# Kernel tuning notes

Hardware: AMD Instinct MI355X
Metric: run time of the kernel (lower is better)

## Reference

```python
import jax, jax.numpy as jnp
import numpy as np

NUM_EMBEDDINGS = 1024
EMBEDDING_DIM = 256
COMMITMENT_COST = 0.25
DECAY = 0.99
EPSILON = 1e-05


def setup_inputs() -> dict:
    key = jax.random.key(0)
    k1, k2, k3 = jax.random.split(key, 3)
    z = jax.random.normal(k1, (32, EMBEDDING_DIM, 32, 32), dtype=jnp.float32)
    codebook = jax.random.normal(k2, (NUM_EMBEDDINGS, EMBEDDING_DIM), dtype=jnp.float32)
    ema_cluster_size = jnp.zeros((NUM_EMBEDDINGS,), dtype=jnp.float32)
    ema_dw = jax.random.normal(k3, (NUM_EMBEDDINGS, EMBEDDING_DIM), dtype=jnp.float32)
    return {"z": z, "codebook": codebook, "ema_cluster_size": ema_cluster_size, "ema_dw": ema_dw}


def reference(z, codebook, ema_cluster_size, ema_dw):
    K, D = codebook.shape
    # (B,C,H,W) -> (B,H,W,C)
    zp = jnp.transpose(z, (0, 2, 3, 1))
    z_flat = zp.reshape(-1, D)  # [N, D]
    N = z_flat.shape[0]

    # squared L2 distances to each code: [N, K]
    distances = (jnp.sum(z_flat ** 2, axis=1, keepdims=True)
                 + jnp.sum(codebook ** 2, axis=1)
                 - 2.0 * z_flat @ codebook.T)
    idx = jnp.argmin(distances, axis=1)  # [N]

    quantized = codebook[idx].reshape(zp.shape)  # [B,H,W,C]

    # training-mode EMA codebook update (one-hot scatter expressed as segment sums)
    counts = jax.ops.segment_sum(jnp.ones((N,), z_flat.dtype), idx, num_segments=K)  # encodings.sum(0)
    dw = jax.ops.segment_sum(z_flat, idx, num_segments=K)                            # encodings.T @ z_flat
    new_cluster_size = ema_cluster_size * DECAY + (1.0 - DECAY) * counts
    new_ema_dw = ema_dw * DECAY + (1.0 - DECAY) * dw
    n = jnp.sum(new_cluster_size)
    cluster_size = (new_cluster_size + EPSILON) / (n + K * EPSILON) * n
    new_codebook = new_ema_dw / cluster_size[:, None]

    commitment_loss = jnp.mean((zp - jax.lax.stop_gradient(quantized)) ** 2)
    loss = COMMITMENT_COST * commitment_loss

    # straight-through estimator
    quantized_st = zp + jax.lax.stop_gradient(quantized - zp)

    avg_probs = counts / N
    perplexity = jnp.exp(-jnp.sum(avg_probs * jnp.log(avg_probs + 1e-10)))

    quantized_out = jnp.transpose(quantized_st, (0, 3, 1, 2))  # back to (B,C,H,W)
    return (quantized_out, loss, perplexity, new_codebook, new_cluster_size, new_ema_dw)
```

## Files before the change

### kernel.cpp

```cpp
#include <hip/hip_runtime.h>
#include <cfloat>
#include <cstdint>

#define B_BATCH 32
#define D_DIM   256
#define HW      1024
#define N_POS   32768
#define K_CODES 1024
#define DECAY_F   0.99f
#define ONE_M_DECAY 0.01f
#define EPS_F   1e-5f

#define OUT_Q    0
#define OUT_LOSS 8388608
#define OUT_PERP 8388609
#define OUT_CB   8388610
#define OUT_NCS  8650754
#define OUT_EDW  8651778


#define WS_COUNTS  0
#define WS_ZNORM   4096
#define WS_BSUM    4100
#define WS_MEMSET  4104
#define WS_CBNORM  4352
#define WS_OFFS    8448
#define WS_CURSOR  12544
#define WS_IDX     16640
#define WS_SORTED  147712
#define WS_CBHI    278784
#define WS_CBLO    803072
#define WS_PART    1327360
#define WS_SCODE   3424512
#define WS_TOTAL   3555584

typedef short s16x8 __attribute__((ext_vector_type(8)));
typedef float f32x4 __attribute__((ext_vector_type(4)));
typedef unsigned long long u64;

__device__ __forceinline__ ushort f2bf_rne(float x) {
    uint u = __float_as_uint(x);
    uint r = (u + 0x7FFF + ((u >> 16) & 1)) >> 16;
    return (ushort)r;
}
__device__ __forceinline__ float bf2f(ushort h) {
    return __uint_as_float(((uint)h) << 16);
}

__device__ __forceinline__ void gload16(const void* g, void* l) {
    __builtin_amdgcn_global_load_lds(
        (const __attribute__((address_space(1))) unsigned*)(uintptr_t)g,
        (__attribute__((address_space(3))) unsigned*)(uintptr_t)l, 16, 0, 0);
}

__global__ __launch_bounds__(256) void prep_ztrans(const float* __restrict__ z,
                                                   const float* __restrict__ cb,
                                                   ushort* __restrict__ zhi,
                                                   ushort* __restrict__ zlo,
                                                   ushort* __restrict__ cbhi,
                                                   ushort* __restrict__ cblo,
                                                   float* __restrict__ cbnorm,
                                                   float* __restrict__ znorm_acc) {
    __shared__ float Zs[32][65];
    __shared__ float red[256];
    const int tid = threadIdx.x;

    if (blockIdx.x >= 512) {
        int wave = tid >> 6;
        int lane = tid & 63;
        int k = (blockIdx.x - 512) * 4 + wave;
        float4 v = *(const float4*)&cb[(size_t)k * D_DIM + lane * 4];
        ushort4 h, l;
        h.x = f2bf_rne(v.x); l.x = f2bf_rne(v.x - bf2f(h.x));
        h.y = f2bf_rne(v.y); l.y = f2bf_rne(v.y - bf2f(h.y));
        h.z = f2bf_rne(v.z); l.z = f2bf_rne(v.z - bf2f(h.z));
        h.w = f2bf_rne(v.w); l.w = f2bf_rne(v.w - bf2f(h.w));
        *(ushort4*)&cbhi[(size_t)k * D_DIM + lane * 4] = h;
        *(ushort4*)&cblo[(size_t)k * D_DIM + lane * 4] = l;
        float s = v.x * v.x + v.y * v.y + v.z * v.z + v.w * v.w;
        #pragma unroll
        for (int off = 32; off >= 1; off >>= 1) s += __shfl_xor(s, off);
        if (lane == 0) cbnorm[k] = s;
        return;
    }

    const int n0  = blockIdx.x * 64;
    const int b   = n0 >> 10;
    const int hw0 = n0 & 1023;
    const float* zb = z + (size_t)b * (D_DIM * HW) + hw0;

    const int zn = tid & 63;
    const int zdb = (tid >> 6) * 8;
    const int n  = tid >> 2;
    const int dq = tid & 3;
    float zsum = 0.f;

    for (int d0 = 0; d0 < D_DIM; d0 += 32) {
        __syncthreads();
        #pragma unroll
        for (int j = 0; j < 8; ++j)
            Zs[zdb + j][zn] = zb[(size_t)(d0 + zdb + j) * HW + zn];
        __syncthreads();
        s16x8 hv, lv;
        #pragma unroll
        for (int j = 0; j < 8; ++j) {
            float f = Zs[dq * 8 + j][n];
            zsum += f * f;
            ushort hb = f2bf_rne(f);
            ushort lb = f2bf_rne(f - bf2f(hb));
            hv[j] = (short)hb;
            lv[j] = (short)lb;
        }
        *(s16x8*)&zhi[(size_t)(n0 + n) * D_DIM + d0 + dq * 8] = hv;
        *(s16x8*)&zlo[(size_t)(n0 + n) * D_DIM + d0 + dq * 8] = lv;
    }
    red[tid] = zsum;
    __syncthreads();
    for (int s2 = 128; s2 >= 1; s2 >>= 1) {
        if (tid < s2) red[tid] += red[tid + s2];
        __syncthreads();
    }
    if (tid == 0) atomicAdd(znorm_acc, red[0]);
}

__global__ __launch_bounds__(512, 2) void argmin_gemm(const ushort* __restrict__ cbhi,
                                                      const ushort* __restrict__ cblo,
                                                      const ushort* __restrict__ zhi,
                                                      const ushort* __restrict__ zlo,
                                                      const float* __restrict__ cbnorm,
                                                      u64* __restrict__ partial) {
    __shared__ __align__(16) ushort lds[73728];

    const int tid  = threadIdx.x;
    const int wave = tid >> 6;
    const int lane = tid & 63;
    const int col  = lane & 15;
    const int lg   = lane >> 4;
    const int wr   = wave >> 1;
    const int wc   = wave & 1;
    const int blk  = blockIdx.x;
    const int mt = (blk >> 3) & 3;
    const int pt = (blk & 7) | ((blk >> 5) << 3);

    const int srow = tid >> 2;
    const int G    = tid & 3;
    const int sg   = (G ^ ((srow >> 1) & 3)) * 16;
    const char* pAh = (const char*)cbhi + (size_t)(mt * 256 + srow) * 512 + sg;
    const char* pAl = (const char*)cblo + (size_t)(mt * 256 + srow) * 512 + sg;
    const char* pBh = (const char*)zhi  + (size_t)(pt * 128 + srow) * 512 + sg;
    const char* pBl = (const char*)zlo  + (size_t)(pt * 128 + srow) * 512 + sg;
    char* const ldsw = (char*)lds + wave * 1024;

    auto stage_a = [&](int kt, int bsel) {
        char* d = ldsw + bsel * 49152;
        const int kb = kt * 64;
        gload16(pAh + kb,         d);
        gload16(pAh + kb + 65536, d + 8192);
        gload16(pBh + kb,         d + 32768);
    };
    auto stage_b = [&](int kt, int bsel) {
        char* d = ldsw + bsel * 49152;
        const int kb = kt * 64;
        gload16(pAl + kb,         d + 16384);
        gload16(pAl + kb + 65536, d + 24576);
        gload16(pBl + kb,         d + 40960);
    };

    const char* ldsc = (const char*)lds;
    const int swz  = (lg ^ ((col >> 1) & 3)) * 16;
    const int aoff = (wr * 64 + col) * 64 + swz;
    const int boff = (wc * 64 + col) * 64 + swz;

    f32x4 acc[4][4];
    #pragma unroll
    for (int mi = 0; mi < 4; ++mi)
        #pragma unroll
        for (int ni = 0; ni < 4; ++ni) acc[mi][ni] = {0.f, 0.f, 0.f, 0.f};

    stage_a(0, 0); stage_b(0, 0);
    stage_a(1, 1); stage_b(1, 1);

#define MM3(mi, ni)                                                                                  \
    acc[mi][ni] = __builtin_amdgcn_mfma_f32_16x16x32_bf16(ah[mi], bh[ni], acc[mi][ni], 0, 0, 0);     \
    acc[mi][ni] = __builtin_amdgcn_mfma_f32_16x16x32_bf16(ah[mi], bl[ni], acc[mi][ni], 0, 0, 0);     \
    acc[mi][ni] = __builtin_amdgcn_mfma_f32_16x16x32_bf16(al[mi], bh[ni], acc[mi][ni], 0, 0, 0);

    #pragma unroll
    for (int t = 0; t < 8; ++t) {
        const int cur = t % 3;
        if (t < 7) asm volatile("s_waitcnt vmcnt(6)" ::: "memory");
        else       asm volatile("s_waitcnt vmcnt(0)" ::: "memory");
        __builtin_amdgcn_s_barrier();
        __builtin_amdgcn_sched_barrier(0);

        const char* bp = ldsc + cur * 49152;
        s16x8 ah[4], al[4], bh[4], bl[4];

        ah[0] = *(const s16x8*)(bp + aoff);
        al[0] = *(const s16x8*)(bp + 16384 + aoff);
        ah[1] = *(const s16x8*)(bp + aoff + 1024);
        al[1] = *(const s16x8*)(bp + 16384 + aoff + 1024);
        bh[0] = *(const s16x8*)(bp + 32768 + boff);
        bl[0] = *(const s16x8*)(bp + 40960 + boff);
        bh[1] = *(const s16x8*)(bp + 32768 + boff + 1024);
        bl[1] = *(const s16x8*)(bp + 40960 + boff + 1024);
        if (t < 6) stage_a(t + 2, (t + 2) % 3);
        __builtin_amdgcn_s_setprio(1);
        MM3(0, 0) MM3(0, 1) MM3(1, 0) MM3(1, 1)
        __builtin_amdgcn_s_setprio(0);

        bh[2] = *(const s16x8*)(bp + 32768 + boff + 2048);
        bl[2] = *(const s16x8*)(bp + 40960 + boff + 2048);
        bh[3] = *(const s16x8*)(bp + 32768 + boff + 3072);
        bl[3] = *(const s16x8*)(bp + 40960 + boff + 3072);
        if (t < 6) stage_b(t + 2, (t + 2) % 3);
        __builtin_amdgcn_s_setprio(1);
        MM3(0, 2) MM3(0, 3) MM3(1, 2) MM3(1, 3)
        __builtin_amdgcn_s_setprio(0);

        ah[2] = *(const s16x8*)(bp + aoff + 2048);
        al[2] = *(const s16x8*)(bp + 16384 + aoff + 2048);
        ah[3] = *(const s16x8*)(bp + aoff + 3072);
        al[3] = *(const s16x8*)(bp + 16384 + aoff + 3072);
        __builtin_amdgcn_s_setprio(1);
        MM3(2, 2) MM3(2, 3) MM3(3, 2) MM3(3, 3)
        __builtin_amdgcn_s_setprio(0);

        __builtin_amdgcn_s_setprio(1);
        MM3(2, 0) MM3(2, 1) MM3(3, 0) MM3(3, 1)
        __builtin_amdgcn_s_setprio(0);
    }
#undef MM3

    const int kbase = mt * 256 + wr * 64;
    u64 best[4] = {~0ull, ~0ull, ~0ull, ~0ull};
    #pragma unroll
    for (int mi = 0; mi < 4; ++mi) {
        float4 cn = *(const float4*)&cbnorm[kbase + mi * 16 + lg * 4];
        const float* cnp = (const float*)&cn;
        #pragma unroll
        for (int ni = 0; ni < 4; ++ni) {
            #pragma unroll
            for (int r = 0; r < 4; ++r) {
                float dist = cnp[r] - 2.f * acc[mi][ni][r];
                uint ub = __float_as_uint(dist);
                ub = ub ^ (uint)(((int)ub >> 31) | 0x80000000);
                u64 key = ((u64)ub << 32) | (uint)(kbase + mi * 16 + lg * 4 + r);
                if (key < best[ni]) best[ni] = key;
            }
        }
    }
    #pragma unroll
    for (int ni = 0; ni < 4; ++ni) {
        u64 o = __shfl_xor(best[ni], 16); if (o < best[ni]) best[ni] = o;
        o = __shfl_xor(best[ni], 32); if (o < best[ni]) best[ni] = o;
    }
    u64* kredp = (u64*)lds;
    if (lane < 16) {
        #pragma unroll
        for (int ni = 0; ni < 4; ++ni)
            kredp[(wc * 64 + ni * 16 + lane) * 4 + wr] = best[ni];
    }
    __syncthreads();
    if (tid < 128) {
        u64 a = kredp[tid * 4 + 0];
        u64 b = kredp[tid * 4 + 1]; if (b < a) a = b;
        b = kredp[tid * 4 + 2]; if (b < a) a = b;
        b = kredp[tid * 4 + 3]; if (b < a) a = b;
        partial[(size_t)(pt * 128 + tid) * 4 + mt] = a;
    }
}

__global__ __launch_bounds__(256) void combine_kernel(const u64* __restrict__ partial,
                                                      int* __restrict__ idx,
                                                      float* __restrict__ counts,
                                                      float* __restrict__ bsum_acc) {
    __shared__ int hist[1024];
    __shared__ float red[256];
    const int tid = threadIdx.x;
    for (int j = tid; j < 1024; j += 256) hist[j] = 0;
    __syncthreads();
    int n = blockIdx.x * 256 + tid;
    const u64* p = partial + (size_t)n * 4;
    u64 m = p[0];
    #pragma unroll
    for (int j = 1; j < 4; ++j) { u64 v = p[j]; if (v < m) m = v; }
    int k = (int)(m & 1023u);
    idx[n] = k;
    atomicAdd(&hist[k], 1);
    uint ub = (uint)(m >> 32);
    uint u = (ub & 0x80000000u) ? (ub ^ 0x80000000u) : ~ub;
    red[tid] = __uint_as_float(u);
    __syncthreads();
    for (int s2 = 128; s2 >= 1; s2 >>= 1) {
        if (tid < s2) red[tid] += red[tid + s2];
        __syncthreads();
    }
    if (tid == 0) atomicAdd(bsum_acc, red[0]);
    for (int j = tid; j < 1024; j += 256) {
        int c = hist[j];
        if (c) atomicAdd(&counts[j], (float)c);
    }
}

__global__ __launch_bounds__(1024) void small_kernel(const float* __restrict__ ema_cs,
                                                     const float* __restrict__ counts,
                                                     const float* __restrict__ znorm,
                                                     const float* __restrict__ bsum,
                                                     float* __restrict__ out_ncs,
                                                     float* __restrict__ out_perp,
                                                     float* __restrict__ out_loss,
                                                     float* __restrict__ ntot_ws,
                                                     int* __restrict__ offsets,
                                                     int* __restrict__ cursor) {
    __shared__ float s1[1024];
    __shared__ float s2[1024];
    __shared__ int   s3[1024];
    int k = threadIdx.x;
    float cnt = counts[k];
    float ncs = ema_cs[k] * DECAY_F + ONE_M_DECAY * cnt;
    out_ncs[k] = ncs;
    float p = cnt / (float)N_POS;
    s1[k] = ncs;
    s2[k] = p * logf(p + 1e-10f);
    int c = (int)cnt;
    s3[k] = c;
    __syncthreads();
    for (int off = 1; off < 1024; off <<= 1) {
        int v = (k >= off) ? s3[k - off] : 0;
        __syncthreads();
        s3[k] += v;
        __syncthreads();
    }
    int excl = s3[k] - c;
    offsets[k] = excl;
    cursor[k] = excl;
    for (int st = 512; st >= 1; st >>= 1) {
        if (k < st) { s1[k] += s1[k + st]; s2[k] += s2[k + st]; }
        __syncthreads();
    }
    if (k == 0) {
        ntot_ws[0] = s1[0];
        out_perp[0] = expf(-s2[0]);
        out_loss[0] = 0.25f * (znorm[0] + bsum[0]) / 8388608.0f;
    }
}

__global__ __launch_bounds__(256) void scatter_kernel(const int* __restrict__ idx,
                                                      int* __restrict__ cursor,
                                                      int* __restrict__ sorted,
                                                      int* __restrict__ scode,
                                                      float* __restrict__ dw_zero) {
    __shared__ int hist[1024];
    __shared__ int base_s[1024];
    const int tid = threadIdx.x;
    {
        float4 z4 = {0.f, 0.f, 0.f, 0.f};
        size_t e = ((size_t)blockIdx.x * 256 + tid) * 8;
        *(float4*)&dw_zero[e] = z4;
        *(float4*)&dw_zero[e + 4] = z4;
    }
    for (int j = tid; j < 1024; j += 256) hist[j] = 0;
    __syncthreads();
    int n = blockIdx.x * 256 + tid;
    int k = idx[n];
    atomicAdd(&hist[k], 1);
    __syncthreads();
    for (int j = tid; j < 1024; j += 256) {
        int c = hist[j];
        if (c) base_s[j] = atomicAdd(&cursor[j], c);
        hist[j] = 0;
    }
    __syncthreads();
    int rank = atomicAdd(&hist[k], 1);
    int pos = base_s[k] + rank;
    sorted[pos] = n;
    scode[pos] = k;
}

#define DW_CHUNK 64
__global__ __launch_bounds__(256) void dw_chunk_kernel(const ushort* __restrict__ zhi,
                                                       const ushort* __restrict__ zlo,
                                                       const int* __restrict__ sorted,
                                                       const int* __restrict__ scode,
                                                       const int* __restrict__ offsets,
                                                       const float* __restrict__ counts,
                                                       float* __restrict__ dw) {
    __shared__ int sid[DW_CHUNK];
    __shared__ int sk[DW_CHUNK];
    const int tid = threadIdx.x;
    const int p0 = blockIdx.x * DW_CHUNK;
    if (tid < DW_CHUNK) {
        sid[tid] = sorted[p0 + tid];
        sk[tid]  = scode[p0 + tid];
    }
    __syncthreads();
    float acc = 0.f;
    int runstart = 0;
    #pragma unroll 4
    for (int i = 0; i < DW_CHUNK; ++i) {
        int id = sid[i];
        float zv = bf2f(zhi[(size_t)id * D_DIM + tid]) + bf2f(zlo[(size_t)id * D_DIM + tid]);
        acc += zv;
        bool end = (i == DW_CHUNK - 1) || (sk[i + 1] != sk[i]);
        if (end) {
            int k = sk[i];
            int off = offsets[k];
            int cnt = (int)counts[k];
            if (p0 + runstart == off && p0 + i == off + cnt - 1)
                dw[(size_t)k * D_DIM + tid] = acc;
            else
                atomicAdd(&dw[(size_t)k * D_DIM + tid], acc);
            acc = 0.f;
            runstart = i + 1;
        }
    }
}

__global__ __launch_bounds__(256) void tail_fused(const float* __restrict__ cb,
                                                  const int* __restrict__ idx,
                                                  float* __restrict__ outq,
                                                  const float* __restrict__ ema_dw,
                                                  const float* __restrict__ out_ncs,
                                                  const float* __restrict__ ntot_ws,
                                                  float* __restrict__ out_edw,
                                                  float* __restrict__ out_cb) {
    const int tid = threadIdx.x;
    if (blockIdx.x >= 512) {
        int k = blockIdx.x - 512;
        int d = tid;
        float ncs = out_ncs[k];
        float nt = ntot_ws[0];
        float csz = (ncs + EPS_F) / (nt + (float)K_CODES * EPS_F) * nt;
        size_t e = (size_t)k * D_DIM + d;
        float ed = ema_dw[e] * DECAY_F + ONE_M_DECAY * out_edw[e];
        out_edw[e] = ed;
        out_cb[e] = ed / csz;
        return;
    }

    __shared__ float Qs[32][65];
    __shared__ int kidx[64];
    const int n0  = blockIdx.x * 64;
    const int b   = n0 >> 10;
    const int hw0 = n0 & 1023;
    float* ob = outq + (size_t)b * (D_DIM * HW) + hw0;

    if (tid < 64) kidx[tid] = idx[n0 + tid];

    for (int d0 = 0; d0 < D_DIM; d0 += 32) {
        __syncthreads();
        #pragma unroll
        for (int h = 0; h < 2; ++h) {
            int s  = tid + 256 * h;
            int n  = s >> 3;
            int dq = s & 7;
            int k  = kidx[n];
            float4 q = *(const float4*)&cb[(size_t)k * D_DIM + d0 + dq * 4];
            Qs[dq * 4 + 0][n] = q.x;
            Qs[dq * 4 + 1][n] = q.y;
            Qs[dq * 4 + 2][n] = q.z;
            Qs[dq * 4 + 3][n] = q.w;
        }
        __syncthreads();
        #pragma unroll
        for (int j = 0; j < 8; ++j) {
            int v = tid + 256 * j;
            int d = v >> 6;
            int n = v & 63;
            ob[(size_t)(d0 + d) * HW + n] = Qs[d][n];
        }
    }
}

extern "C" void kernel_launch(void* const* d_in, const int* in_sizes, int n_in,
                              void* d_out, int out_size, void* d_ws, size_t ws_size,
                              hipStream_t stream) {
    const float* z       = (const float*)d_in[0];
    const float* cb      = (const float*)d_in[1];
    const float* ema_cs  = (const float*)d_in[2];
    const float* ema_dw  = (const float*)d_in[3];
    float* out = (float*)d_out;

    char* ws = (char*)d_ws;
    float* ws_counts = (float*)(ws + WS_COUNTS);
    float* ws_znorm  = (float*)(ws + WS_ZNORM);
    float* ws_bsum   = (float*)(ws + WS_BSUM);
    float* ws_cbnorm = (float*)(ws + WS_CBNORM);
    int*   ws_offs   = (int*)(ws + WS_OFFS);
    int*   ws_cursor = (int*)(ws + WS_CURSOR);
    int*   ws_idx    = (int*)(ws + WS_IDX);
    int*   ws_sorted = (int*)(ws + WS_SORTED);
    ushort* ws_cbhi  = (ushort*)(ws + WS_CBHI);
    ushort* ws_cblo  = (ushort*)(ws + WS_CBLO);
    u64*   ws_part   = (u64*)(ws + WS_PART);
    int*   ws_scode  = (int*)(ws + WS_SCODE);

    ushort* zhi = (ushort*)out;
    ushort* zlo = zhi + 8388608;

    hipMemsetAsync(d_ws, 0, WS_MEMSET, stream);

    prep_ztrans<<<768, 256, 0, stream>>>(z, cb, zhi, zlo, ws_cbhi, ws_cblo,
                                         ws_cbnorm, ws_znorm);
    argmin_gemm<<<1024, 512, 0, stream>>>(ws_cbhi, ws_cblo, zhi, zlo, ws_cbnorm, ws_part);
    combine_kernel<<<N_POS / 256, 256, 0, stream>>>(ws_part, ws_idx, ws_counts, ws_bsum);
    small_kernel<<<1, 1024, 0, stream>>>(ema_cs, ws_counts, ws_znorm, ws_bsum,
                                         out + OUT_NCS, out + OUT_PERP, out + OUT_LOSS,
                                         (float*)(ws + WS_ZNORM) + 1024, ws_offs, ws_cursor);
    scatter_kernel<<<N_POS / 256, 256, 0, stream>>>(ws_idx, ws_cursor, ws_sorted,
                                                    ws_scode, out + OUT_EDW);
    dw_chunk_kernel<<<N_POS / DW_CHUNK, 256, 0, stream>>>(zhi, zlo, ws_sorted, ws_scode,
                                                          ws_offs, ws_counts, out + OUT_EDW);
    tail_fused<<<1536, 256, 0, stream>>>(cb, ws_idx, out + OUT_Q, ema_dw, out + OUT_NCS,
                                         (float*)(ws + WS_ZNORM) + 1024,
                                         out + OUT_EDW, out + OUT_CB);
}
```

Baseline: 204.8 us.

## Enlarge argmin GEMM tile to 256x256 with double-buffered LDS staging

Each argmin_gemm block now covers 256 positions instead of 128. Waves are rearranged 2x4, each computing a 128x64 sub-tile with an 8x4 accumulator array. This halves the grid and raises reuse of the codebook tile loaded into LDS. The triple-buffered 96KB pipeline with partial vmcnt waits becomes a 128KB double buffer: four quarter-stages of loads interleaved with compute, and a full vmcnt(0) wait each iteration. The trade-off is higher register pressure, which could cause spills under launch_bounds(512,2), and more LDS per block, likely one block per CU. That means less latency hiding and fewer blocks to fill the machine.

Result: faster. 196.7 us (-3.9%).

```diff
diff --git a/kernel.cpp b/kernel.cpp
--- a/kernel.cpp
+++ b/kernel.cpp
@@ -129,15 +129,15 @@
                                                       const ushort* __restrict__ zlo,
                                                       const float* __restrict__ cbnorm,
                                                       u64* __restrict__ partial) {
-    __shared__ __align__(16) ushort lds[73728];
+    __shared__ __align__(16) ushort lds[65536];
 
     const int tid  = threadIdx.x;
     const int wave = tid >> 6;
     const int lane = tid & 63;
     const int col  = lane & 15;
     const int lg   = lane >> 4;
-    const int wr   = wave >> 1;
-    const int wc   = wave & 1;
+    const int wr   = wave >> 2;
+    const int wc   = wave & 3;
     const int blk  = blockIdx.x;
     const int mt = (blk >> 3) & 3;
     const int pt = (blk & 7) | ((blk >> 5) << 3);
@@ -147,95 +147,100 @@
     const int sg   = (G ^ ((srow >> 1) & 3)) * 16;
     const char* pAh = (const char*)cbhi + (size_t)(mt * 256 + srow) * 512 + sg;
     const char* pAl = (const char*)cblo + (size_t)(mt * 256 + srow) * 512 + sg;
-    const char* pBh = (const char*)zhi  + (size_t)(pt * 128 + srow) * 512 + sg;
-    const char* pBl = (const char*)zlo  + (size_t)(pt * 128 + srow) * 512 + sg;
+    const char* pBh = (const char*)zhi  + (size_t)(pt * 256 + srow) * 512 + sg;
+    const char* pBl = (const char*)zlo  + (size_t)(pt * 256 + srow) * 512 + sg;
     char* const ldsw = (char*)lds + wave * 1024;
 
-    auto stage_a = [&](int kt, int bsel) {
-        char* d = ldsw + bsel * 49152;
+    auto stage_q = [&](int kt, int bsel, int q) {
+        char* d = ldsw + bsel * 65536;
         const int kb = kt * 64;
-        gload16(pAh + kb,         d);
-        gload16(pAh + kb + 65536, d + 8192);
-        gload16(pBh + kb,         d + 32768);
-    };
-    auto stage_b = [&](int kt, int bsel) {
-        char* d = ldsw + bsel * 49152;
-        const int kb = kt * 64;
-        gload16(pAl + kb,         d + 16384);
-        gload16(pAl + kb + 65536, d + 24576);
-        gload16(pBl + kb,         d + 40960);
+        if (q == 0)      { gload16(pAh + kb, d);         gload16(pAh + kb + 65536, d + 8192);  }
+        else if (q == 1) { gload16(pAl + kb, d + 16384); gload16(pAl + kb + 65536, d + 24576); }
+        else if (q == 2) { gload16(pBh + kb, d + 32768); gload16(pBh + kb + 65536, d + 40960); }
+        else             { gload16(pBl + kb, d + 49152); gload16(pBl + kb + 65536, d + 57344); }
     };
 
     const char* ldsc = (const char*)lds;
     const int swz  = (lg ^ ((col >> 1) & 3)) * 16;
-    const int aoff = (wr * 64 + col) * 64 + swz;
+    const int aoff = (wr * 128 + col) * 64 + swz;
     const int boff = (wc * 64 + col) * 64 + swz;
 
-    f32x4 acc[4][4];
+    f32x4 acc[8][4];
     #pragma unroll
-    for (int mi = 0; mi < 4; ++mi)
+    for (int mi = 0; mi < 8; ++mi)
         #pragma unroll
         for (int ni = 0; ni < 4; ++ni) acc[mi][ni] = {0.f, 0.f, 0.f, 0.f};
 
-    stage_a(0, 0); stage_b(0, 0);
-    stage_a(1, 1); stage_b(1, 1);
-
-#define MM3(mi, ni)                                                                                  \
-    acc[mi][ni] = __builtin_amdgcn_mfma_f32_16x16x32_bf16(ah[mi], bh[ni], acc[mi][ni], 0, 0, 0);     \
-    acc[mi][ni] = __builtin_amdgcn_mfma_f32_16x16x32_bf16(ah[mi], bl[ni], acc[mi][ni], 0, 0, 0);     \
-    acc[mi][ni] = __builtin_amdgcn_mfma_f32_16x16x32_bf16(al[mi], bh[ni], acc[mi][ni], 0, 0, 0);
+    stage_q(0, 0, 0); stage_q(0, 0, 1); stage_q(0, 0, 2); stage_q(0, 0, 3);
+
+#define MM3A(AH, AL, mi, ni)                                                                   \
+    acc[mi][ni] = __builtin_amdgcn_mfma_f32_16x16x32_bf16(AH, bh[ni], acc[mi][ni], 0, 0, 0);   \
+    acc[mi][ni] = __builtin_amdgcn_mfma_f32_16x16x32_bf16(AH, bl[ni], acc[mi][ni], 0, 0, 0);   \
+    acc[mi][ni] = __builtin_amdgcn_mfma_f32_16x16x32_bf16(AL, bh[ni], acc[mi][ni], 0, 0, 0);
+#define ROW3(AH, AL, mi) MM3A(AH, AL, mi, 0) MM3A(AH, AL, mi, 1) MM3A(AH, AL, mi, 2) MM3A(AH, AL, mi, 3)
 
     #pragma unroll
     for (int t = 0; t < 8; ++t) {
-        const int cur = t % 3;
-        if (t < 7) asm volatile("s_waitcnt vmcnt(6)" ::: "memory");
-        else       asm volatile("s_waitcnt vmcnt(0)" ::: "memory");
+        asm volatile("s_waitcnt vmcnt(0)" ::: "memory");
         __builtin_amdgcn_s_barrier();
         __builtin_amdgcn_sched_barrier(0);
 
-        const char* bp = ldsc + cur * 49152;
-        s16x8 ah[4], al[4], bh[4], bl[4];
-
-        ah[0] = *(const s16x8*)(bp + aoff);
-        al[0] = *(const s16x8*)(bp + 16384 + aoff);
-        ah[1] = *(const s16x8*)(bp + aoff + 1024);
-        al[1] = *(const s16x8*)(bp + 16384 + aoff + 1024);
+        const char* bp = ldsc + (t & 1) * 65536;
+        const int nb = (t + 1) & 1;
+        s16x8 bh[4], bl[4];
+        s16x8 ah0, al0, ah1, al1;
+
         bh[0] = *(const s16x8*)(bp + 32768 + boff);
-        bl[0] = *(const s16x8*)(bp + 40960 + boff);
+        bl[0] = *(const s16x8*)(bp + 49152 + boff);
         bh[1] = *(const s16x8*)(bp + 32768 + boff + 1024);
-        bl[1] = *(const s16x8*)(bp + 40960 + boff + 1024);
-        if (t < 6) stage_a(t + 2, (t + 2) % 3);
+        bl[1] = *(const s16x8*)(bp + 49152 + boff + 1024);
+        bh[2] = *(const s16x8*)(bp + 32768 + boff + 2048);
+        bl[2] = *(const s16x8*)(bp + 49152 + boff + 2048);
+        bh[3] = *(const s16x8*)(bp + 32768 + boff + 3072);
+        bl[3] = *(const s16x8*)(bp + 49152 + boff + 3072);
+        ah0 = *(const s16x8*)(bp + aoff);
+        al0 = *(const s16x8*)(bp + 16384 + aoff);
+        ah1 = *(const s16x8*)(bp + aoff + 1024);
+        al1 = *(const s16x8*)(bp + 16384 + aoff + 1024);
+        if (t < 7) stage_q(t + 1, nb, 0);
         __builtin_amdgcn_s_setprio(1);
-        MM3(0, 0) MM3(0, 1) MM3(1, 0) MM3(1, 1)
+        ROW3(ah0, al0, 0) ROW3(ah1, al1, 1)
         __builtin_amdgcn_s_setprio(0);
 
-        bh[2] = *(const s16x8*)(bp + 32768 + boff + 2048);
-        bl[2] = *(const s16x8*)(bp + 40960 + boff + 2048);
-        bh[3] = *(const s16x8*)(bp + 32768 + boff + 3072);
-        bl[3] = *(const s16x8*)(bp + 40960 + boff + 3072);
-        if (t < 6) stage_b(t + 2, (t + 2) % 3);
+        ah0 = *(const s16x8*)(bp + aoff + 2048);
+        al0 = *(const s16x8*)(bp + 16384 + aoff + 2048);
+        ah1 = *(const s16x8*)(bp + aoff + 3072);
+        al1 = *(const s16x8*)(bp + 16384 + aoff + 3072);
+        if (t < 7) stage_q(t + 1, nb, 1);
         __builtin_amdgcn_s_setprio(1);
-        MM3(0, 2) MM3(0, 3) MM3(1, 2) MM3(1, 3)
+        ROW3(ah0, al0, 2) ROW3(ah1, al1, 3)
         __builtin_amdgcn_s_setprio(0);
 
-        ah[2] = *(const s16x8*)(bp + aoff + 2048);
-        al[2] = *(const s16x8*)(bp + 16384 + aoff + 2048);
-        ah[3] = *(const s16x8*)(bp + aoff + 3072);
-        al[3] = *(const s16x8*)(bp + 16384 + aoff + 3072);
+        ah0 = *(const s16x8*)(bp + aoff + 4096);
+        al0 = *(const s16x8*)(bp + 16384 + aoff + 4096);
+        ah1 = *(const s16x8*)(bp + aoff + 5120);
+        al1 = *(const s16x8*)(bp + 16384 + aoff + 5120);
+        if (t < 7) stage_q(t + 1, nb, 2);
         __builtin_amdgcn_s_setprio(1);
-        MM3(2, 2) MM3(2, 3) MM3(3, 2) MM3(3, 3)
+        ROW3(ah0, al0, 4) ROW3(ah1, al1, 5)
         __builtin_amdgcn_s_setprio(0);
 
+        ah0 = *(const s16x8*)(bp + aoff + 6144);
+        al0 = *(const s16x8*)(bp + 16384 + aoff + 6144);
+        ah1 = *(const s16x8*)(bp + aoff + 7168);
+        al1 = *(const s16x8*)(bp + 16384 + aoff + 7168);
+        if (t < 7) stage_q(t + 1, nb, 3);
         __builtin_amdgcn_s_setprio(1);
-        MM3(2, 0) MM3(2, 1) MM3(3, 0) MM3(3, 1)
+        ROW3(ah0, al0, 6) ROW3(ah1, al1, 7)
         __builtin_amdgcn_s_setprio(0);
     }
-#undef MM3
-
-    const int kbase = mt * 256 + wr * 64;
+#undef ROW3
+#undef MM3A
+
+    const int kbase = mt * 256 + wr * 128;
     u64 best[4] = {~0ull, ~0ull, ~0ull, ~0ull};
     #pragma unroll
-    for (int mi = 0; mi < 4; ++mi) {
+    for (int mi = 0; mi < 8; ++mi) {
         float4 cn = *(const float4*)&cbnorm[kbase + mi * 16 + lg * 4];
         const float* cnp = (const float*)&cn;
         #pragma unroll
@@ -259,15 +264,13 @@
     if (lane < 16) {
         #pragma unroll
         for (int ni = 0; ni < 4; ++ni)
-            kredp[(wc * 64 + ni * 16 + lane) * 4 + wr] = best[ni];
-    }
-    __syncthreads();
-    if (tid < 128) {
-        u64 a = kredp[tid * 4 + 0];
-        u64 b = kredp[tid * 4 + 1]; if (b < a) a = b;
-        b = kredp[tid * 4 + 2]; if (b < a) a = b;
-        b = kredp[tid * 4 + 3]; if (b < a) a = b;
-        partial[(size_t)(pt * 128 + tid) * 4 + mt] = a;
+            kredp[(wc * 64 + ni * 16 + lane) * 2 + wr] = best[ni];
+    }
+    __syncthreads();
+    if (tid < 256) {
+        u64 a = kredp[tid * 2 + 0];
+        u64 b = kredp[tid * 2 + 1]; if (b < a) a = b;
+        partial[(size_t)(pt * 256 + tid) * 4 + mt] = a;
     }
 }
 
@@ -503,7 +506,7 @@
 
     prep_ztrans<<<768, 256, 0, stream>>>(z, cb, zhi, zlo, ws_cbhi, ws_cblo,
                                          ws_cbnorm, ws_znorm);
-    argmin_gemm<<<1024, 512, 0, stream>>>(ws_cbhi, ws_cblo, zhi, zlo, ws_cbnorm, ws_part);
+    argmin_gemm<<<512, 512, 0, stream>>>(ws_cbhi, ws_cblo, zhi, zlo, ws_cbnorm, ws_part);
     combine_kernel<<<N_POS / 256, 256, 0, stream>>>(ws_part, ws_idx, ws_counts, ws_bsum);
     small_kernel<<<1, 1024, 0, stream>>>(ema_cs, ws_counts, ws_znorm, ws_bsum,
                                          out + OUT_NCS, out + OUT_PERP, out + OUT_LOSS,
```
